# Performance work log

Measured on AMD Instinct MI355X. Metric: run time of the kernel, lower is better.

Reference implementation:

```python
import jax, jax.numpy as jnp
import numpy as np

N, B, M, D, K = 131072, 1024, 128, 256, 32
T1 = 0.1
GAMMA = 0.99
BN_EPS = 1e-5
LRELU_SLOPE = 0.01


def setup_inputs() -> dict:
    key = jax.random.key(0)
    ks = jax.random.split(key, 8)
    z = jax.random.normal(ks[0], (N, D), dtype=jnp.float32)
    g = jax.random.normal(ks[1], (B, D), dtype=jnp.float32)
    batch = (jnp.arange(N, dtype=jnp.int32) // M)  # B graphs, M nodes each
    W1 = jax.random.normal(ks[2], (D, D), dtype=jnp.float32) / np.sqrt(D)
    b1 = jnp.zeros((D,), jnp.float32)
    bn_gamma = jnp.ones((D,), jnp.float32)
    bn_beta = jnp.zeros((D,), jnp.float32)
    W2 = jax.random.normal(ks[3], (D, K), dtype=jnp.float32) / np.sqrt(D)
    b2 = jnp.zeros((K,), jnp.float32)
    U = jax.random.uniform(ks[4], (K, D), dtype=jnp.float32, minval=-1.5, maxval=1.5)
    return {"z": z, "g": g, "batch": batch, "W1": W1, "b1": b1,
            "bn_gamma": bn_gamma, "bn_beta": bn_beta, "W2": W2, "b2": b2, "U": U}


def _to_dense_batch(x, batch, num_graphs, max_nodes):
    # PyG to_dense_batch: scatter nodes into [B, M, ...] padded tensor + mask
    n = x.shape[0]
    counts = jax.ops.segment_sum(jnp.ones((n,), jnp.int32), batch, num_segments=num_graphs)
    offsets = jnp.concatenate([jnp.zeros((1,), jnp.int32), jnp.cumsum(counts)[:-1]])
    pos = jnp.arange(n, dtype=jnp.int32) - offsets[batch]  # index within graph
    dense = jnp.zeros((num_graphs, max_nodes) + x.shape[1:], x.dtype).at[batch, pos].set(x)
    mask = jnp.zeros((num_graphs, max_nodes), bool).at[batch, pos].set(True)
    return dense, mask


def reference(z, g, batch, W1, b1, bn_gamma, bn_beta, W2, b2, U):
    # node_classifier: Linear -> BatchNorm1d (train-mode batch stats) -> LeakyReLU -> Linear
    h1 = z @ W1 + b1
    mu = h1.mean(0)
    var = h1.var(0)  # biased, as BN normalization
    h1 = (h1 - mu) / jnp.sqrt(var + BN_EPS) * bn_gamma + bn_beta
    h1 = jnp.where(h1 > 0, h1, LRELU_SLOPE * h1)
    logits = h1 @ W2 + b2  # [N, K]
    s = jax.nn.softmax(logits / T1, axis=-1)

    z_dense, _ = _to_dense_batch(z, batch, B, M)        # [B, M, D]
    s_dense, _ = _to_dense_batch(s, batch, B, M)        # [B, M, K]

    # std-based sub-cluster filter (torch.std is unbiased, ddof=1, over cluster dim)
    std = jnp.std(s_dense, axis=-1, ddof=1, keepdims=True)
    sub_filter = s_dense > (std + 1.0 / K)
    s_dense = s_dense * sub_filter.astype(s_dense.dtype)

    p_hat = s_dense.sum(axis=1)                          # [B, K]
    p_hat = p_hat / (p_hat + 1e-12)
    p_hat = p_hat[:, :, None] * jnp.eye(K, dtype=p_hat.dtype)  # diag_embed -> [B, K, K]

    # L1-normalized soft-cluster pooling
    w = jnp.swapaxes(s_dense, 1, 2)                      # [B, K, M]
    w = w / jnp.maximum(jnp.abs(w).sum(-1, keepdims=True), 1e-12)
    h_dense = jnp.einsum('bkm,bmd->bkd', w, z_dense)     # [B, K, D]
    sub_mask = jnp.abs(h_dense).sum(-1) > 0.0            # [B, K]

    # EMA centroid update (note: original uses .view(K, B), a reshape, not transpose)
    h_perm = jnp.transpose(h_dense, (1, 0, 2))           # [K, B, D]
    mask_r = sub_mask.reshape(K, B)
    sizes = mask_r.astype(h_perm.dtype).sum(-1, keepdims=True)  # [K, 1]
    centroids = h_perm.sum(axis=1) / (sizes + 1e-10)
    centroids = jax.lax.stop_gradient(centroids)
    U_new = GAMMA * U + (1.0 - GAMMA) * centroids        # [K, D]

    # h = h_dense[sub_mask] has dynamic shape; return flat h with masked rows zeroed
    h_flat = h_dense.reshape(B * K, D) * sub_mask.reshape(-1, 1).astype(h_dense.dtype)
    hn = h_flat / jnp.maximum(jnp.linalg.norm(h_flat, axis=-1, keepdims=True), 1e-12)
    Un = U / jnp.maximum(jnp.linalg.norm(U, axis=-1, keepdims=True), 1e-12)
    p = hn @ Un.T                                        # [B*K, K] pairwise cos sim

    return (s, h_flat, h_dense, p, p_hat, z_dense, g, sub_mask, U_new)
```

## Files before the change

kernel.cpp:

```cpp
#include <hip/hip_runtime.h>
#include <math.h>

#define NN 131072
#define BBG 1024
#define MMN 128
#define DDF 256
#define KKC 32

#define OFF_S      0
#define OFF_HFLAT  4194304
#define OFF_HDENSE 12582912
#define OFF_P      20971520
#define OFF_PHAT   22020096
#define OFF_ZD     23068672
#define OFF_G      56623104
#define OFF_MASK   56885248
#define OFF_UNEW   56918016

#define WS_PSUM  0
#define WS_PSQ   524288
#define WS_TMP   1048576
#define WS_SCALE 1052672
#define WS_SHIFT 1052928
#define WS_UN    1053184
#define WS_SF    1061376
#define WS_C     5255680
#define WS_PART  5288448

typedef __attribute__((ext_vector_type(8))) short short8;
typedef __attribute__((ext_vector_type(4))) float f32x4;

__device__ __forceinline__ unsigned short f2bf(float x) {
  unsigned u = __float_as_uint(x);
  u += 0x7fffu + ((u >> 16) & 1u);
  return (unsigned short)(u >> 16);
}
__device__ __forceinline__ float bf2f(unsigned short h) {
  return __uint_as_float(((unsigned)h) << 16);
}

__global__ __launch_bounds__(256) void k0_prep(const float* __restrict__ W1,
    unsigned short* __restrict__ preh, unsigned short* __restrict__ prel)
{
  int tid = blockIdx.x * 256 + threadIdx.x;
  int n = tid & 255, kq = tid >> 8;
  short8 hv, lv;
  #pragma unroll
  for (int j = 0; j < 8; ++j) {
    float v = W1[(kq * 8 + j) * DDF + n];
    unsigned short hb = f2bf(v);
    hv[j] = (short)hb;
    lv[j] = (short)f2bf(v - bf2f(hb));
  }
  int base = (kq >> 2) * 8192 + (kq & 3) * 2048 + n * 8;
  *(short8*)(preh + base) = hv;
  *(short8*)(prel + base) = lv;
}

__device__ __forceinline__ void cvt_storeA(float4 za, float4 zb,
    unsigned short* AhB, unsigned short* AlB, int arow, int ac)
{
  unsigned short h0 = f2bf(za.x), h1v = f2bf(za.y), h2 = f2bf(za.z), h3 = f2bf(za.w);
  unsigned short g0 = f2bf(zb.x), g1 = f2bf(zb.y), g2 = f2bf(zb.z), g3 = f2bf(zb.w);
  uint2 hA = make_uint2((unsigned)h0 | ((unsigned)h1v << 16),
                        (unsigned)h2 | ((unsigned)h3 << 16));
  uint2 hB = make_uint2((unsigned)g0 | ((unsigned)g1 << 16),
                        (unsigned)g2 | ((unsigned)g3 << 16));
  uint2 lA = make_uint2((unsigned)f2bf(za.x - bf2f(h0)) | ((unsigned)f2bf(za.y - bf2f(h1v)) << 16),
                        (unsigned)f2bf(za.z - bf2f(h2)) | ((unsigned)f2bf(za.w - bf2f(h3)) << 16));
  uint2 lB = make_uint2((unsigned)f2bf(zb.x - bf2f(g0)) | ((unsigned)f2bf(zb.y - bf2f(g1)) << 16),
                        (unsigned)f2bf(zb.z - bf2f(g2)) | ((unsigned)f2bf(zb.w - bf2f(g3)) << 16));
  *(uint2*)(AhB + arow * 40 + ac * 4)      = hA;
  *(uint2*)(AhB + arow * 40 + 16 + ac * 4) = hB;
  *(uint2*)(AlB + arow * 40 + ac * 4)      = lA;
  *(uint2*)(AlB + arow * 40 + 16 + ac * 4) = lB;
}

__global__ __launch_bounds__(512) void k1_gemm1(
    const float* __restrict__ z, const unsigned short* __restrict__ preh,
    const unsigned short* __restrict__ prel, const float* __restrict__ b1,
    float* __restrict__ h1, float* __restrict__ psum, float* __restrict__ psq)
{
  __shared__ __attribute__((aligned(16))) unsigned short Ah[2 * 128 * 40];
  __shared__ __attribute__((aligned(16))) unsigned short Al[2 * 128 * 40];

  const int t = threadIdx.x;
  const int l = t & 63;
  const int w = t >> 6;
  const int wr = w >> 2;
  const int wc = w & 3;
  const int lg = l >> 4;
  const int l16 = l & 15;
  const int n0 = blockIdx.x * 128;

  f32x4 acc[4][4];
  #pragma unroll
  for (int i = 0; i < 4; ++i)
    #pragma unroll
    for (int j = 0; j < 4; ++j) acc[i][j] = (f32x4)0.0f;

  const int arow = t >> 2, ac = t & 3;
  const float* zrow = z + (size_t)(n0 + arow) * DDF;
  const unsigned short* bhbase = preh + lg * 2048 + wc * 512 + l16 * 8;
  const unsigned short* blbase = prel + lg * 2048 + wc * 512 + l16 * 8;

  {
    float4 za = *(const float4*)(zrow + ac * 4);
    float4 zb = *(const float4*)(zrow + 16 + ac * 4);
    cvt_storeA(za, zb, Ah, Al, arow, ac);
  }

  #pragma unroll
  for (int ks = 0; ks < 8; ++ks) {
    const int cur = (ks & 1) * 5120;
    const int nxt = 5120 - cur;
    float4 za, zb;
    if (ks < 7) {
      za = *(const float4*)(zrow + (ks + 1) * 32 + ac * 4);
      zb = *(const float4*)(zrow + (ks + 1) * 32 + 16 + ac * 4);
    }
    short8 bfh[4], bfl[4];
    #pragma unroll
    for (int nf = 0; nf < 4; ++nf) {
      bfh[nf] = *(const short8*)(bhbase + ks * 8192 + nf * 128);
      bfl[nf] = *(const short8*)(blbase + ks * 8192 + nf * 128);
    }
    asm volatile("s_waitcnt lgkmcnt(0)" ::: "memory");
    __builtin_amdgcn_s_barrier();
    __builtin_amdgcn_sched_barrier(0);
    #pragma unroll
    for (int mf = 0; mf < 4; ++mf) {
      const int ar = wr * 64 + mf * 16 + l16;
      short8 afh = *(const short8*)(&Ah[cur + ar * 40 + lg * 8]);
      short8 afl = *(const short8*)(&Al[cur + ar * 40 + lg * 8]);
      #pragma unroll
      for (int nf = 0; nf < 4; ++nf) {
        acc[mf][nf] = __builtin_amdgcn_mfma_f32_16x16x32_bf16(afh, bfh[nf], acc[mf][nf], 0, 0, 0);
        acc[mf][nf] = __builtin_amdgcn_mfma_f32_16x16x32_bf16(afh, bfl[nf], acc[mf][nf], 0, 0, 0);
        acc[mf][nf] = __builtin_amdgcn_mfma_f32_16x16x32_bf16(afl, bfh[nf], acc[mf][nf], 0, 0, 0);
        acc[mf][nf] = __builtin_amdgcn_mfma_f32_16x16x32_bf16(afl, bfl[nf], acc[mf][nf], 0, 0, 0);
      }
    }
    if (ks < 7) cvt_storeA(za, zb, Ah + nxt, Al + nxt, arow, ac);
  }

  float s1[4] = {0, 0, 0, 0}, s2[4] = {0, 0, 0, 0};
  #pragma unroll
  for (int nf = 0; nf < 4; ++nf) {
    int c = wc * 64 + nf * 16 + l16;
    float bb = b1[c];
    #pragma unroll
    for (int mf = 0; mf < 4; ++mf) {
      int rbase = n0 + wr * 64 + mf * 16 + lg * 4;
      #pragma unroll
      for (int j = 0; j < 4; ++j) {
        float v = acc[mf][nf][j] + bb;
        s1[nf] += v; s2[nf] += v * v;
        h1[(size_t)(rbase + j) * DDF + c] = v;
      }
    }
  }
  #pragma unroll
  for (int nf = 0; nf < 4; ++nf) {
    s1[nf] += __shfl_xor(s1[nf], 16); s1[nf] += __shfl_xor(s1[nf], 32);
    s2[nf] += __shfl_xor(s2[nf], 16); s2[nf] += __shfl_xor(s2[nf], 32);
  }
  __syncthreads();
  float* red1 = (float*)Ah;
  float* red2 = (float*)Al;
  if (l < 16) {
    #pragma unroll
    for (int nf = 0; nf < 4; ++nf) {
      red1[wr * 256 + wc * 64 + nf * 16 + l] = s1[nf];
      red2[wr * 256 + wc * 64 + nf * 16 + l] = s2[nf];
    }
  }
  __syncthreads();
  if (t < 256) {
    psum[blockIdx.x * 256 + t] = red1[t] + red1[256 + t];
    psq [blockIdx.x * 256 + t] = red2[t] + red2[256 + t];
  }
}

__global__ __launch_bounds__(256) void k2a(const float* __restrict__ psum,
                                           const float* __restrict__ psq,
                                           float* __restrict__ tmp)
{
  int g = blockIdx.x & 7;
  const float* src = (blockIdx.x < 8) ? psum : psq;
  float acc = 0.f;
  #pragma unroll 8
  for (int r = 0; r < 128; ++r) acc += src[(g * 128 + r) * 256 + threadIdx.x];
  tmp[blockIdx.x * 256 + threadIdx.x] = acc;
}

__global__ __launch_bounds__(256) void k2b(const float* __restrict__ tmp,
    const float* __restrict__ gam, const float* __restrict__ bet,
    float* __restrict__ scale, float* __restrict__ shift)
{
  int d = threadIdx.x;
  float s1 = 0.f, s2 = 0.f;
  #pragma unroll
  for (int g = 0; g < 8; ++g) { s1 += tmp[g*256+d]; s2 += tmp[(8+g)*256+d]; }
  float mu  = s1 * (1.0f / (float)NN);
  float var = s2 * (1.0f / (float)NN) - mu*mu;
  float inv = 1.0f / sqrtf(var + 1e-5f);
  float sc = gam[d] * inv;
  scale[d] = sc;
  shift[d] = bet[d] - mu*sc;
}

__global__ __launch_bounds__(64) void k2c(const float* __restrict__ U,
                                          float* __restrict__ Un)
{
  int k = blockIdx.x, l = threadIdx.x;
  float4 u = *(const float4*)(U + k*256 + l*4);
  float ss = u.x*u.x + u.y*u.y + u.z*u.z + u.w*u.w;
  #pragma unroll
  for (int off = 32; off >= 1; off >>= 1) ss += __shfl_xor(ss, off);
  float inv = 1.0f / fmaxf(sqrtf(ss), 1e-12f);
  *(float4*)(Un + k*256 + l*4) = make_float4(u.x*inv, u.y*inv, u.z*inv, u.w*inv);
}

__global__ __launch_bounds__(256) void k3_gemm2(
    const float* __restrict__ h1, const float* __restrict__ W2,
    const float* __restrict__ b2, const float* __restrict__ scale,
    const float* __restrict__ shift, float* __restrict__ s_out,
    float* __restrict__ sf_out)
{
  __shared__ float ylds[4][128*32];
  const int t = threadIdx.x;
  const int w = t >> 6, l = t & 63;
  const int b = blockIdx.x*4 + w;
  float* my = ylds[w];

  float acc0[32], acc1[32];
  #pragma unroll
  for (int k = 0; k < 32; ++k) { acc0[k] = 0.f; acc1[k] = 0.f; }

  const int slot  = l & 7;
  const int rbase = l >> 3;
  const int lx7   = l & 7;

  for (int ch = 0; ch < 8; ++ch) {
    const int dbase = ch*32 + slot*4;
    const float4 sc = *(const float4*)(scale + dbase);
    const float4 sh = *(const float4*)(shift + dbase);
    #pragma unroll
    for (int i = 0; i < 16; ++i) {
      int row = rbase + i*8;
      float4 v = *(const float4*)(h1 + (size_t)(b*MMN + row)*DDF + dbase);
      float y0 = fmaf(v.x, sc.x, sh.x); y0 = y0 > 0.f ? y0 : 0.01f*y0;
      float y1 = fmaf(v.y, sc.y, sh.y); y1 = y1 > 0.f ? y1 : 0.01f*y1;
      float y2 = fmaf(v.z, sc.z, sh.z); y2 = y2 > 0.f ? y2 : 0.01f*y2;
      float y3 = fmaf(v.w, sc.w, sh.w); y3 = y3 > 0.f ? y3 : 0.01f*y3;
      *(float4*)(&my[row*32 + (slot ^ (row & 7))*4]) = make_float4(y0,y1,y2,y3);
    }
    #pragma unroll
    for (int d4 = 0; d4 < 8; ++d4) {
      float4 ya = *(const float4*)(&my[ l     *32 + ((d4 ^ lx7))*4]);
      float4 yb = *(const float4*)(&my[(l+64)*32 + ((d4 ^ lx7))*4]);
      #pragma unroll
      for (int dd = 0; dd < 4; ++dd) {
        const float* w2r = W2 + (ch*32 + d4*4 + dd)*KKC;
        float a = (dd==0?ya.x: dd==1?ya.y: dd==2?ya.z: ya.w);
        float c = (dd==0?yb.x: dd==1?yb.y: dd==2?yb.z: yb.w);
        #pragma unroll
        for (int k = 0; k < 32; ++k) {
          float wv = w2r[k];
          acc0[k] = fmaf(a, wv, acc0[k]);
          acc1[k] = fmaf(c, wv, acc1[k]);
        }
      }
    }
  }
  #pragma unroll
  for (int k = 0; k < 32; ++k) {
    float bb = b2[k];
    acc0[k] = (acc0[k] + bb) * 10.0f;
    acc1[k] = (acc1[k] + bb) * 10.0f;
  }
  float thr0, thr1;
  {
    float* a = acc0; float* thrp = &thr0;
    #pragma unroll
    for (int r = 0; r < 2; ++r) {
      float m = a[0];
      #pragma unroll
      for (int k = 1; k < 32; ++k) m = fmaxf(m, a[k]);
      float sum = 0.f;
      #pragma unroll
      for (int k = 0; k < 32; ++k) { float e = expf(a[k]-m); a[k] = e; sum += e; }
      float inv = 1.0f/sum;
      float ssum = 0.f;
      #pragma unroll
      for (int k = 0; k < 32; ++k) { a[k] *= inv; ssum += a[k]; }
      float mean = ssum * (1.0f/32.0f);
      float var = 0.f;
      #pragma unroll
      for (int k = 0; k < 32; ++k) { float d = a[k]-mean; var += d*d; }
      *thrp = sqrtf(var * (1.0f/31.0f)) + 0.03125f;
      a = acc1; thrp = &thr1;
    }
  }
  #pragma unroll
  for (int q = 0; q < 8; ++q) {
    *(float4*)(&my[ l     *32 + (q ^ lx7)*4]) =
        make_float4(acc0[q*4],acc0[q*4+1],acc0[q*4+2],acc0[q*4+3]);
    *(float4*)(&my[(l+64)*32 + (q ^ lx7)*4]) =
        make_float4(acc1[q*4],acc1[q*4+1],acc1[q*4+2],acc1[q*4+3]);
  }
  #pragma unroll
  for (int i = 0; i < 16; ++i) {
    int fid = l + i*64;
    int row = fid >> 3, q = fid & 7;
    *(float4*)(s_out + (size_t)b*4096 + fid*4) =
        *(const float4*)(&my[row*32 + (q ^ (row & 7))*4]);
  }
  #pragma unroll
  for (int k = 0; k < 32; ++k) {
    acc0[k] = acc0[k] > thr0 ? acc0[k] : 0.f;
    acc1[k] = acc1[k] > thr1 ? acc1[k] : 0.f;
  }
  #pragma unroll
  for (int q = 0; q < 8; ++q) {
    *(float4*)(&my[ l     *32 + (q ^ lx7)*4]) =
        make_float4(acc0[q*4],acc0[q*4+1],acc0[q*4+2],acc0[q*4+3]);
    *(float4*)(&my[(l+64)*32 + (q ^ lx7)*4]) =
        make_float4(acc1[q*4],acc1[q*4+1],acc1[q*4+2],acc1[q*4+3]);
  }
  #pragma unroll
  for (int i = 0; i < 16; ++i) {
    int fid = l + i*64;
    int row = fid >> 3, q = fid & 7;
    *(float4*)(sf_out + (size_t)b*4096 + fid*4) =
        *(const float4*)(&my[row*32 + (q ^ (row & 7))*4]);
  }
}

__global__ __launch_bounds__(256) void k4_pool(
    const float* __restrict__ sf, const float* __restrict__ z,
    const float* __restrict__ Un, float* __restrict__ c_out,
    float* __restrict__ hdense, float* __restrict__ hflat,
    float* __restrict__ p_out, float* __restrict__ mask_out,
    float* __restrict__ zd)
{
  __shared__ __align__(16) char smem[66048];
  __shared__ float redp[8*32];
  __shared__ float cred[32];
  float* sflds = (float*)smem;
  float* zlds  = (float*)(smem + 16384);
  float* hnlds = (float*)smem;
  float* unlds = (float*)(smem + 33280);

  const int t = threadIdx.x;
  const int w = t >> 6, l = t & 63;
  const int b = blockIdx.x;

  #pragma unroll
  for (int i = 0; i < 4; ++i) {
    int fid = t + i*256;
    *(float4*)(&sflds[fid*4]) = *(const float4*)(sf + (size_t)b*4096 + fid*4);
  }
  __syncthreads();
  {
    int k = t & 31, mg = t >> 5;
    float p = 0.f;
    #pragma unroll
    for (int m = 0; m < 16; ++m) p += sflds[(mg*16+m)*32 + k];
    redp[mg*32 + k] = p;
  }
  __syncthreads();
  if (t < 32) {
    float c = 0.f;
    #pragma unroll
    for (int g = 0; g < 8; ++g) c += redp[g*32 + t];
    cred[t] = c;
    c_out[b*32 + t] = c;
  }
  __syncthreads();

  float acc[8][4];
  #pragma unroll
  for (int kk = 0; kk < 8; ++kk)
    #pragma unroll
    for (int j = 0; j < 4; ++j) acc[kk][j] = 0.f;

  for (int ch = 0; ch < 4; ++ch) {
    #pragma unroll
    for (int i = 0; i < 8; ++i) {
      int fid = t + i*256;
      float4 v = *(const float4*)(z + (size_t)(b*128 + ch*32)*256 + fid*4);
      *(float4*)(&zlds[fid*4]) = v;
      *(float4*)(zd + (size_t)(b*128 + ch*32)*256 + fid*4) = v;
    }
    __syncthreads();
    #pragma unroll
    for (int mm = 0; mm < 32; ++mm) {
      float4 zv = *(const float4*)(&zlds[mm*256 + l*4]);
      float4 sa = *(const float4*)(&sflds[(ch*32+mm)*32 + w*8]);
      float4 sb = *(const float4*)(&sflds[(ch*32+mm)*32 + w*8 + 4]);
      float sv[8] = {sa.x,sa.y,sa.z,sa.w,sb.x,sb.y,sb.z,sb.w};
      #pragma unroll
      for (int kk = 0; kk < 8; ++kk) {
        acc[kk][0] = fmaf(sv[kk], zv.x, acc[kk][0]);
        acc[kk][1] = fmaf(sv[kk], zv.y, acc[kk][1]);
        acc[kk][2] = fmaf(sv[kk], zv.z, acc[kk][2]);
        acc[kk][3] = fmaf(sv[kk], zv.w, acc[kk][3]);
      }
    }
    __syncthreads();
  }
  float asum[8], qsum[8], mkarr[8];
  #pragma unroll
  for (int kk = 0; kk < 8; ++kk) {
    float wnv = 1.0f / fmaxf(cred[w*8+kk], 1e-12f);
    acc[kk][0]*=wnv; acc[kk][1]*=wnv; acc[kk][2]*=wnv; acc[kk][3]*=wnv;
    asum[kk] = fabsf(acc[kk][0])+fabsf(acc[kk][1])+fabsf(acc[kk][2])+fabsf(acc[kk][3]);
    qsum[kk] = acc[kk][0]*acc[kk][0]+acc[kk][1]*acc[kk][1]
             + acc[kk][2]*acc[kk][2]+acc[kk][3]*acc[kk][3];
  }
  #pragma unroll
  for (int kk = 0; kk < 8; ++kk) {
    float a = asum[kk], q = qsum[kk];
    #pragma unroll
    for (int off = 1; off < 64; off <<= 1) {
      a += __shfl_xor(a, off); q += __shfl_xor(q, off);
    }
    asum[kk] = a; qsum[kk] = q;
  }
  #pragma unroll
  for (int kk = 0; kk < 8; ++kk) {
    int krow = b*32 + w*8 + kk;
    float mk = asum[kk] > 0.f ? 1.0f : 0.0f;
    mkarr[kk] = mk;
    float inv = 1.0f / fmaxf(sqrtf(qsum[kk]) * mk, 1e-12f);
    float h0=acc[kk][0], h1v=acc[kk][1], h2=acc[kk][2], h3=acc[kk][3];
    *(float4*)(hdense + (size_t)krow*256 + l*4) = make_float4(h0,h1v,h2,h3);
    float f0=h0*mk, f1=h1v*mk, f2=h2*mk, f3=h3*mk;
    *(float4*)(hflat + (size_t)krow*256 + l*4) = make_float4(f0,f1,f2,f3);
    acc[kk][0]=f0*inv; acc[kk][1]=f1*inv; acc[kk][2]=f2*inv; acc[kk][3]=f3*inv;
  }
  if (l == 0) {
    #pragma unroll
    for (int kk = 0; kk < 8; ++kk) mask_out[b*32 + w*8 + kk] = mkarr[kk];
  }
  #pragma unroll
  for (int kk = 0; kk < 8; ++kk)
    *(float4*)(&hnlds[(w*8+kk)*260 + l*4]) =
        make_float4(acc[kk][0],acc[kk][1],acc[kk][2],acc[kk][3]);
  #pragma unroll
  for (int i = 0; i < 8; ++i) {
    int fid = t + i*256;
    *(float4*)(&unlds[fid*4]) = *(const float4*)(Un + fid*4);
  }
  __syncthreads();
  {
    const int k = t & 31, k2 = (t >> 5) * 4;
    float p0=0.f, p1=0.f, p2=0.f, p3=0.f;
    #pragma unroll 8
    for (int d4 = 0; d4 < 64; ++d4) {
      float4 hv = *(const float4*)(&hnlds[k*260 + d4*4]);
      float4 u0 = *(const float4*)(&unlds[(k2+0)*256 + d4*4]);
      float4 u1 = *(const float4*)(&unlds[(k2+1)*256 + d4*4]);
      float4 u2 = *(const float4*)(&unlds[(k2+2)*256 + d4*4]);
      float4 u3 = *(const float4*)(&unlds[(k2+3)*256 + d4*4]);
      p0 = fmaf(hv.x,u0.x,fmaf(hv.y,u0.y,fmaf(hv.z,u0.z,fmaf(hv.w,u0.w,p0))));
      p1 = fmaf(hv.x,u1.x,fmaf(hv.y,u1.y,fmaf(hv.z,u1.z,fmaf(hv.w,u1.w,p1))));
      p2 = fmaf(hv.x,u2.x,fmaf(hv.y,u2.y,fmaf(hv.z,u2.z,fmaf(hv.w,u2.w,p2))));
      p3 = fmaf(hv.x,u3.x,fmaf(hv.y,u3.y,fmaf(hv.z,u3.z,fmaf(hv.w,u3.w,p3))));
    }
    *(float4*)(p_out + (size_t)(b*32 + k)*32 + k2) = make_float4(p0,p1,p2,p3);
  }
}

__global__ __launch_bounds__(256) void k5a(const float* __restrict__ hdense,
                                           float* __restrict__ part)
{
  int k = blockIdx.x & 31, seg = blockIdx.x >> 5;
  int t = threadIdx.x;
  float s = 0.f;
  #pragma unroll 4
  for (int i = 0; i < 128; ++i) {
    int b = seg*128 + i;
    s += hdense[(size_t)(b*32 + k)*256 + t];
  }
  part[blockIdx.x*256 + t] = s;
}

__global__ __launch_bounds__(256) void k5b(const float* __restrict__ part,
    const float* __restrict__ maskf, const float* __restrict__ U,
    float* __restrict__ Unew)
{
  __shared__ float r4[4];
  int k = blockIdx.x, t = threadIdx.x;
  float4 mv = *(const float4*)(maskf + k*1024 + t*4);
  float m4 = mv.x + mv.y + mv.z + mv.w;
  #pragma unroll
  for (int off = 1; off < 64; off <<= 1) m4 += __shfl_xor(m4, off);
  if ((t & 63) == 0) r4[t >> 6] = m4;
  __syncthreads();
  float sizes = r4[0] + r4[1] + r4[2] + r4[3];
  float csum = 0.f;
  #pragma unroll
  for (int g = 0; g < 8; ++g) csum += part[(g*32 + k)*256 + t];
  float cent = csum / (sizes + 1e-10f);
  Unew[k*256 + t] = 0.99f * U[k*256 + t] + 0.01f * cent;
}

__global__ __launch_bounds__(256) void k6_phat(const float* __restrict__ c,
                                               float* __restrict__ phat)
{
  int idx = blockIdx.x*256 + threadIdx.x;
  int b = idx >> 10, rr = idx & 1023, k1 = rr >> 5, k2 = rr & 31;
  float v = 0.f;
  if (k1 == k2) { float cc = c[b*32 + k1]; v = cc / (cc + 1e-12f); }
  phat[idx] = v;
}

__global__ __launch_bounds__(256) void k7_copy(const float* __restrict__ g,
                                               float* __restrict__ gout)
{
  int idx = blockIdx.x*256 + threadIdx.x;
  *(float4*)(gout + (size_t)idx*4) = *(const float4*)(g + (size_t)idx*4);
}

extern "C" void kernel_launch(void* const* d_in, const int* in_sizes, int n_in,
                              void* d_out, int out_size, void* d_ws, size_t ws_size,
                              hipStream_t stream)
{
  const float* z   = (const float*)d_in[0];
  const float* g   = (const float*)d_in[1];
  const float* W1  = (const float*)d_in[3];
  const float* b1  = (const float*)d_in[4];
  const float* gam = (const float*)d_in[5];
  const float* bet = (const float*)d_in[6];
  const float* W2  = (const float*)d_in[7];
  const float* b2  = (const float*)d_in[8];
  const float* U   = (const float*)d_in[9];
  float* out = (float*)d_out;
  float* ws  = (float*)d_ws;

  float* h1 = out + OFF_ZD;
  unsigned short* preh = (unsigned short*)(out + OFF_S);
  unsigned short* prel = preh + 65536;

  k0_prep<<<32, 256, 0, stream>>>(W1, preh, prel);
  k1_gemm1<<<1024, 512, 0, stream>>>(z, preh, prel, b1, h1, ws+WS_PSUM, ws+WS_PSQ);
  k2a<<<16, 256, 0, stream>>>(ws+WS_PSUM, ws+WS_PSQ, ws+WS_TMP);
  k2b<<<1, 256, 0, stream>>>(ws+WS_TMP, gam, bet, ws+WS_SCALE, ws+WS_SHIFT);
  k2c<<<32, 64, 0, stream>>>(U, ws+WS_UN);
  k3_gemm2<<<256, 256, 0, stream>>>(h1, W2, b2, ws+WS_SCALE, ws+WS_SHIFT,
                                    out+OFF_S, ws+WS_SF);
  k4_pool<<<1024, 256, 0, stream>>>(ws+WS_SF, z, ws+WS_UN, ws+WS_C,
                                    out+OFF_HDENSE, out+OFF_HFLAT,
                                    out+OFF_P, out+OFF_MASK, out+OFF_ZD);
  k5a<<<256, 256, 0, stream>>>(out+OFF_HDENSE, ws+WS_PART);
  k5b<<<32, 256, 0, stream>>>(ws+WS_PART, out+OFF_MASK, U, out+OFF_UNEW);
  k6_phat<<<4096, 256, 0, stream>>>(ws+WS_C, out+OFF_PHAT);
  k7_copy<<<256, 256, 0, stream>>>(g, out+OFF_G);
}
```

Measured before the change: 327.2 us.

## Drop low-low MFMA term, deepen prefetch, split gemm2 rows, fuse phat/g copy into pool

In gemm1 the z prefetch now runs two k-steps ahead and the MFMA block gets raised priority. The lo*lo bf16 correction product is dropped, leaving three MFMAs per tile instead of four, which slightly lowers the precision of the split-bf16 emulation. gemm2 now gives each wave 64 rows instead of 128, doubling the grid and halving accumulator registers. The pool kernel software-pipelines its z loads, and the phat and g-copy work moves into it so two kernel launches go away.

After: 371.8 us. 1.14x slower.

```diff
diff --git a/kernel.cpp b/kernel.cpp
--- a/kernel.cpp
+++ b/kernel.cpp
@@ -29,6 +29,9 @@
 
 typedef __attribute__((ext_vector_type(8))) short short8;
 typedef __attribute__((ext_vector_type(4))) float f32x4;
+
+#define LGKM_BAR() do { asm volatile("s_waitcnt lgkmcnt(0)" ::: "memory"); \
+  __builtin_amdgcn_s_barrier(); __builtin_amdgcn_sched_barrier(0); } while (0)
 
 __device__ __forceinline__ unsigned short f2bf(float x) {
   unsigned u = __float_as_uint(x);
@@ -109,15 +112,17 @@
     float4 zb = *(const float4*)(zrow + 16 + ac * 4);
     cvt_storeA(za, zb, Ah, Al, arow, ac);
   }
+  float4 zaN = *(const float4*)(zrow + 32 + ac * 4);
+  float4 zbN = *(const float4*)(zrow + 48 + ac * 4);
 
   #pragma unroll
   for (int ks = 0; ks < 8; ++ks) {
     const int cur = (ks & 1) * 5120;
     const int nxt = 5120 - cur;
-    float4 za, zb;
-    if (ks < 7) {
-      za = *(const float4*)(zrow + (ks + 1) * 32 + ac * 4);
-      zb = *(const float4*)(zrow + (ks + 1) * 32 + 16 + ac * 4);
+    float4 zaF, zbF;
+    if (ks < 6) {
+      zaF = *(const float4*)(zrow + (ks + 2) * 32 + ac * 4);
+      zbF = *(const float4*)(zrow + (ks + 2) * 32 + 16 + ac * 4);
     }
     short8 bfh[4], bfl[4];
     #pragma unroll
@@ -125,9 +130,8 @@
       bfh[nf] = *(const short8*)(bhbase + ks * 8192 + nf * 128);
       bfl[nf] = *(const short8*)(blbase + ks * 8192 + nf * 128);
     }
-    asm volatile("s_waitcnt lgkmcnt(0)" ::: "memory");
-    __builtin_amdgcn_s_barrier();
-    __builtin_amdgcn_sched_barrier(0);
+    LGKM_BAR();
+    __builtin_amdgcn_s_setprio(1);
     #pragma unroll
     for (int mf = 0; mf < 4; ++mf) {
       const int ar = wr * 64 + mf * 16 + l16;
@@ -136,12 +140,15 @@
       #pragma unroll
       for (int nf = 0; nf < 4; ++nf) {
         acc[mf][nf] = __builtin_amdgcn_mfma_f32_16x16x32_bf16(afh, bfh[nf], acc[mf][nf], 0, 0, 0);
+        acc[mf][nf] = __builtin_amdgcn_mfma_f32_16x16x32_bf16(afl, bfh[nf], acc[mf][nf], 0, 0, 0);
         acc[mf][nf] = __builtin_amdgcn_mfma_f32_16x16x32_bf16(afh, bfl[nf], acc[mf][nf], 0, 0, 0);
-        acc[mf][nf] = __builtin_amdgcn_mfma_f32_16x16x32_bf16(afl, bfh[nf], acc[mf][nf], 0, 0, 0);
-        acc[mf][nf] = __builtin_amdgcn_mfma_f32_16x16x32_bf16(afl, bfl[nf], acc[mf][nf], 0, 0, 0);
       }
     }
-    if (ks < 7) cvt_storeA(za, zb, Ah + nxt, Al + nxt, arow, ac);
+    __builtin_amdgcn_s_setprio(0);
+    if (ks < 7) {
+      cvt_storeA(zaN, zbN, Ah + nxt, Al + nxt, arow, ac);
+      zaN = zaF; zbN = zbF;
+    }
   }
 
   float s1[4] = {0, 0, 0, 0}, s2[4] = {0, 0, 0, 0};
@@ -228,112 +235,87 @@
     const float* __restrict__ shift, float* __restrict__ s_out,
     float* __restrict__ sf_out)
 {
-  __shared__ float ylds[4][128*32];
+  __shared__ float ylds[4][64*32];
   const int t = threadIdx.x;
   const int w = t >> 6, l = t & 63;
-  const int b = blockIdx.x*4 + w;
+  const int b = blockIdx.x * 2 + (w >> 1);
+  const int half = w & 1;
+  const int rowbase = b * MMN + half * 64;
   float* my = ylds[w];
-
-  float acc0[32], acc1[32];
-  #pragma unroll
-  for (int k = 0; k < 32; ++k) { acc0[k] = 0.f; acc1[k] = 0.f; }
-
-  const int slot  = l & 7;
-  const int rbase = l >> 3;
-  const int lx7   = l & 7;
+  const int lx7 = l & 7;
+  const int rsub = l >> 3;
+
+  float acc[32];
+  #pragma unroll
+  for (int k = 0; k < 32; ++k) acc[k] = 0.f;
 
   for (int ch = 0; ch < 8; ++ch) {
-    const int dbase = ch*32 + slot*4;
-    const float4 sc = *(const float4*)(scale + dbase);
-    const float4 sh = *(const float4*)(shift + dbase);
-    #pragma unroll
-    for (int i = 0; i < 16; ++i) {
-      int row = rbase + i*8;
-      float4 v = *(const float4*)(h1 + (size_t)(b*MMN + row)*DDF + dbase);
+    const float4 sc = *(const float4*)(scale + ch*32 + lx7*4);
+    const float4 sh = *(const float4*)(shift + ch*32 + lx7*4);
+    #pragma unroll
+    for (int i = 0; i < 8; ++i) {
+      int row = rsub + i*8;
+      float4 v = *(const float4*)(h1 + (size_t)(rowbase + row)*DDF + ch*32 + lx7*4);
       float y0 = fmaf(v.x, sc.x, sh.x); y0 = y0 > 0.f ? y0 : 0.01f*y0;
       float y1 = fmaf(v.y, sc.y, sh.y); y1 = y1 > 0.f ? y1 : 0.01f*y1;
       float y2 = fmaf(v.z, sc.z, sh.z); y2 = y2 > 0.f ? y2 : 0.01f*y2;
       float y3 = fmaf(v.w, sc.w, sh.w); y3 = y3 > 0.f ? y3 : 0.01f*y3;
-      *(float4*)(&my[row*32 + (slot ^ (row & 7))*4]) = make_float4(y0,y1,y2,y3);
+      *(float4*)(&my[row*32 + (lx7 ^ rsub)*4]) = make_float4(y0,y1,y2,y3);
     }
     #pragma unroll
     for (int d4 = 0; d4 < 8; ++d4) {
-      float4 ya = *(const float4*)(&my[ l     *32 + ((d4 ^ lx7))*4]);
-      float4 yb = *(const float4*)(&my[(l+64)*32 + ((d4 ^ lx7))*4]);
+      float4 ya = *(const float4*)(&my[l*32 + (d4 ^ lx7)*4]);
       #pragma unroll
       for (int dd = 0; dd < 4; ++dd) {
         const float* w2r = W2 + (ch*32 + d4*4 + dd)*KKC;
         float a = (dd==0?ya.x: dd==1?ya.y: dd==2?ya.z: ya.w);
-        float c = (dd==0?yb.x: dd==1?yb.y: dd==2?yb.z: yb.w);
         #pragma unroll
-        for (int k = 0; k < 32; ++k) {
-          float wv = w2r[k];
-          acc0[k] = fmaf(a, wv, acc0[k]);
-          acc1[k] = fmaf(c, wv, acc1[k]);
-        }
+        for (int k = 0; k < 32; ++k) acc[k] = fmaf(a, w2r[k], acc[k]);
       }
     }
   }
   #pragma unroll
-  for (int k = 0; k < 32; ++k) {
-    float bb = b2[k];
-    acc0[k] = (acc0[k] + bb) * 10.0f;
-    acc1[k] = (acc1[k] + bb) * 10.0f;
-  }
-  float thr0, thr1;
+  for (int k = 0; k < 32; ++k) acc[k] = (acc[k] + b2[k]) * 10.0f;
+  float thr;
   {
-    float* a = acc0; float* thrp = &thr0;
-    #pragma unroll
-    for (int r = 0; r < 2; ++r) {
-      float m = a[0];
-      #pragma unroll
-      for (int k = 1; k < 32; ++k) m = fmaxf(m, a[k]);
-      float sum = 0.f;
-      #pragma unroll
-      for (int k = 0; k < 32; ++k) { float e = expf(a[k]-m); a[k] = e; sum += e; }
-      float inv = 1.0f/sum;
-      float ssum = 0.f;
-      #pragma unroll
-      for (int k = 0; k < 32; ++k) { a[k] *= inv; ssum += a[k]; }
-      float mean = ssum * (1.0f/32.0f);
-      float var = 0.f;
-      #pragma unroll
-      for (int k = 0; k < 32; ++k) { float d = a[k]-mean; var += d*d; }
-      *thrp = sqrtf(var * (1.0f/31.0f)) + 0.03125f;
-      a = acc1; thrp = &thr1;
-    }
-  }
-  #pragma unroll
-  for (int q = 0; q < 8; ++q) {
-    *(float4*)(&my[ l     *32 + (q ^ lx7)*4]) =
-        make_float4(acc0[q*4],acc0[q*4+1],acc0[q*4+2],acc0[q*4+3]);
-    *(float4*)(&my[(l+64)*32 + (q ^ lx7)*4]) =
-        make_float4(acc1[q*4],acc1[q*4+1],acc1[q*4+2],acc1[q*4+3]);
-  }
-  #pragma unroll
-  for (int i = 0; i < 16; ++i) {
+    float m = acc[0];
+    #pragma unroll
+    for (int k = 1; k < 32; ++k) m = fmaxf(m, acc[k]);
+    float sum = 0.f;
+    #pragma unroll
+    for (int k = 0; k < 32; ++k) { float e = expf(acc[k]-m); acc[k] = e; sum += e; }
+    float inv = 1.0f/sum;
+    float ssum = 0.f;
+    #pragma unroll
+    for (int k = 0; k < 32; ++k) { acc[k] *= inv; ssum += acc[k]; }
+    float mean = ssum * (1.0f/32.0f);
+    float var = 0.f;
+    #pragma unroll
+    for (int k = 0; k < 32; ++k) { float d = acc[k]-mean; var += d*d; }
+    thr = sqrtf(var * (1.0f/31.0f)) + 0.03125f;
+  }
+  #pragma unroll
+  for (int q = 0; q < 8; ++q)
+    *(float4*)(&my[l*32 + (q ^ lx7)*4]) =
+        make_float4(acc[q*4],acc[q*4+1],acc[q*4+2],acc[q*4+3]);
+  #pragma unroll
+  for (int i = 0; i < 8; ++i) {
     int fid = l + i*64;
     int row = fid >> 3, q = fid & 7;
-    *(float4*)(s_out + (size_t)b*4096 + fid*4) =
+    *(float4*)(s_out + (size_t)rowbase*KKC + fid*4) =
         *(const float4*)(&my[row*32 + (q ^ (row & 7))*4]);
   }
   #pragma unroll
-  for (int k = 0; k < 32; ++k) {
-    acc0[k] = acc0[k] > thr0 ? acc0[k] : 0.f;
-    acc1[k] = acc1[k] > thr1 ? acc1[k] : 0.f;
-  }
-  #pragma unroll
-  for (int q = 0; q < 8; ++q) {
-    *(float4*)(&my[ l     *32 + (q ^ lx7)*4]) =
-        make_float4(acc0[q*4],acc0[q*4+1],acc0[q*4+2],acc0[q*4+3]);
-    *(float4*)(&my[(l+64)*32 + (q ^ lx7)*4]) =
-        make_float4(acc1[q*4],acc1[q*4+1],acc1[q*4+2],acc1[q*4+3]);
-  }
-  #pragma unroll
-  for (int i = 0; i < 16; ++i) {
+  for (int k = 0; k < 32; ++k) acc[k] = acc[k] > thr ? acc[k] : 0.f;
+  #pragma unroll
+  for (int q = 0; q < 8; ++q)
+    *(float4*)(&my[l*32 + (q ^ lx7)*4]) =
+        make_float4(acc[q*4],acc[q*4+1],acc[q*4+2],acc[q*4+3]);
+  #pragma unroll
+  for (int i = 0; i < 8; ++i) {
     int fid = l + i*64;
     int row = fid >> 3, q = fid & 7;
-    *(float4*)(sf_out + (size_t)b*4096 + fid*4) =
+    *(float4*)(sf_out + (size_t)rowbase*KKC + fid*4) =
         *(const float4*)(&my[row*32 + (q ^ (row & 7))*4]);
   }
 }
@@ -343,7 +325,8 @@
     const float* __restrict__ Un, float* __restrict__ c_out,
     float* __restrict__ hdense, float* __restrict__ hflat,
     float* __restrict__ p_out, float* __restrict__ mask_out,
-    float* __restrict__ zd)
+    float* __restrict__ zd, float* __restrict__ phat,
+    const float* __restrict__ g, float* __restrict__ gout)
 {
   __shared__ __align__(16) char smem[66048];
   __shared__ float redp[8*32];
@@ -357,12 +340,20 @@
   const int w = t >> 6, l = t & 63;
   const int b = blockIdx.x;
 
+  float4 zreg[8];
+  #pragma unroll
+  for (int i = 0; i < 8; ++i) {
+    int fid = t + i*256;
+    zreg[i] = *(const float4*)(z + (size_t)(b*128)*256 + fid*4);
+  }
+  gout[b*256 + t] = g[b*256 + t];
+
   #pragma unroll
   for (int i = 0; i < 4; ++i) {
     int fid = t + i*256;
     *(float4*)(&sflds[fid*4]) = *(const float4*)(sf + (size_t)b*4096 + fid*4);
   }
-  __syncthreads();
+  LGKM_BAR();
   {
     int k = t & 31, mg = t >> 5;
     float p = 0.f;
@@ -370,15 +361,26 @@
     for (int m = 0; m < 16; ++m) p += sflds[(mg*16+m)*32 + k];
     redp[mg*32 + k] = p;
   }
-  __syncthreads();
+  LGKM_BAR();
   if (t < 32) {
     float c = 0.f;
     #pragma unroll
-    for (int g = 0; g < 8; ++g) c += redp[g*32 + t];
+    for (int g2 = 0; g2 < 8; ++g2) c += redp[g2*32 + t];
     cred[t] = c;
     c_out[b*32 + t] = c;
   }
-  __syncthreads();
+  LGKM_BAR();
+  {
+    float cc = cred[t >> 3];
+    float pv = cc / (cc + 1e-12f);
+    int k1r = t >> 3;
+    float4 ph;
+    ph.x = (((t*4+0) & 31) == k1r) ? pv : 0.f;
+    ph.y = (((t*4+1) & 31) == k1r) ? pv : 0.f;
+    ph.z = (((t*4+2) & 31) == k1r) ? pv : 0.f;
+    ph.w = (((t*4+3) & 31) == k1r) ? pv : 0.f;
+    *(float4*)(phat + (size_t)b*1024 + t*4) = ph;
+  }
 
   float acc[8][4];
   #pragma unroll
@@ -387,14 +389,21 @@
     for (int j = 0; j < 4; ++j) acc[kk][j] = 0.f;
 
   for (int ch = 0; ch < 4; ++ch) {
+    float4 znxt[8];
+    if (ch < 3) {
+      #pragma unroll
+      for (int i = 0; i < 8; ++i) {
+        int fid = t + i*256;
+        znxt[i] = *(const float4*)(z + (size_t)(b*128 + (ch+1)*32)*256 + fid*4);
+      }
+    }
     #pragma unroll
     for (int i = 0; i < 8; ++i) {
       int fid = t + i*256;
-      float4 v = *(const float4*)(z + (size_t)(b*128 + ch*32)*256 + fid*4);
-      *(float4*)(&zlds[fid*4]) = v;
-      *(float4*)(zd + (size_t)(b*128 + ch*32)*256 + fid*4) = v;
-    }
-    __syncthreads();
+      *(float4*)(&zlds[fid*4]) = zreg[i];
+      *(float4*)(zd + (size_t)(b*128 + ch*32)*256 + fid*4) = zreg[i];
+    }
+    LGKM_BAR();
     #pragma unroll
     for (int mm = 0; mm < 32; ++mm) {
       float4 zv = *(const float4*)(&zlds[mm*256 + l*4]);
@@ -409,7 +418,11 @@
         acc[kk][3] = fmaf(sv[kk], zv.w, acc[kk][3]);
       }
     }
-    __syncthreads();
+    LGKM_BAR();
+    if (ch < 3) {
+      #pragma unroll
+      for (int i = 0; i < 8; ++i) zreg[i] = znxt[i];
+    }
   }
   float asum[8], qsum[8], mkarr[8];
   #pragma unroll
@@ -454,7 +467,7 @@
     int fid = t + i*256;
     *(float4*)(&unlds[fid*4]) = *(const float4*)(Un + fid*4);
   }
-  __syncthreads();
+  LGKM_BAR();
   {
     const int k = t & 31, k2 = (t >> 5) * 4;
     float p0=0.f, p1=0.f, p2=0.f, p3=0.f;
@@ -508,23 +521,6 @@
   Unew[k*256 + t] = 0.99f * U[k*256 + t] + 0.01f * cent;
 }
 
-__global__ __launch_bounds__(256) void k6_phat(const float* __restrict__ c,
-                                               float* __restrict__ phat)
-{
-  int idx = blockIdx.x*256 + threadIdx.x;
-  int b = idx >> 10, rr = idx & 1023, k1 = rr >> 5, k2 = rr & 31;
-  float v = 0.f;
-  if (k1 == k2) { float cc = c[b*32 + k1]; v = cc / (cc + 1e-12f); }
-  phat[idx] = v;
-}
-
-__global__ __launch_bounds__(256) void k7_copy(const float* __restrict__ g,
-                                               float* __restrict__ gout)
-{
-  int idx = blockIdx.x*256 + threadIdx.x;
-  *(float4*)(gout + (size_t)idx*4) = *(const float4*)(g + (size_t)idx*4);
-}
-
 extern "C" void kernel_launch(void* const* d_in, const int* in_sizes, int n_in,
                               void* d_out, int out_size, void* d_ws, size_t ws_size,
                               hipStream_t stream)
@@ -550,13 +546,12 @@
   k2a<<<16, 256, 0, stream>>>(ws+WS_PSUM, ws+WS_PSQ, ws+WS_TMP);
   k2b<<<1, 256, 0, stream>>>(ws+WS_TMP, gam, bet, ws+WS_SCALE, ws+WS_SHIFT);
   k2c<<<32, 64, 0, stream>>>(U, ws+WS_UN);
-  k3_gemm2<<<256, 256, 0, stream>>>(h1, W2, b2, ws+WS_SCALE, ws+WS_SHIFT,
+  k3_gemm2<<<512, 256, 0, stream>>>(h1, W2, b2, ws+WS_SCALE, ws+WS_SHIFT,
                                     out+OFF_S, ws+WS_SF);
   k4_pool<<<1024, 256, 0, stream>>>(ws+WS_SF, z, ws+WS_UN, ws+WS_C,
                                     out+OFF_HDENSE, out+OFF_HFLAT,
-                                    out+OFF_P, out+OFF_MASK, out+OFF_ZD);
+                                    out+OFF_P, out+OFF_MASK, out+OFF_ZD,
+                                    out+OFF_PHAT, g, out+OFF_G);
   k5a<<<256, 256, 0, stream>>>(out+OFF_HDENSE, ws+WS_PART);
   k5b<<<32, 256, 0, stream>>>(ws+WS_PART, out+OFF_MASK, U, out+OFF_UNEW);
-  k6_phat<<<4096, 256, 0, stream>>>(ws+WS_C, out+OFF_PHAT);
-  k7_copy<<<256, 256, 0, stream>>>(g, out+OFF_G);
-}
+}
```
